# Optimization experiments

Measured on AMD Instinct MI355X. Metric: run time of the kernel, lower is better.

Reference implementation:

```python
import jax, jax.numpy as jnp
import numpy as np

B = 16; SEQ_LEN = 96; PRED_LEN = 96; N_VARS = 862; D_MODEL = 512; D_FF = 1024
N_HEADS = 8; E_LAYERS = 2; D_FREQ = 512; KF_LEN = 5000; ALPHA = 0.5; TOP_P = 0.5
FREQ_DIM = SEQ_LEN // 2 + 1            # rfft bins = 49
KEY_LEN = int(np.ceil(FREQ_DIM * ALPHA))  # 25 -> y_freq in_features = 50
KERNEL = 25; NOISE_EPS = 0.01; LN_EPS = 1e-5; REVIN_EPS = 1e-5


def setup_inputs() -> dict:
    ks = iter(jax.random.split(jax.random.key(0), 64))
    def g(*shape):
        return jax.random.normal(next(ks), shape, jnp.float32) * 0.02
    z = lambda *s: jnp.zeros(s, jnp.float32)
    o = lambda *s: jnp.ones(s, jnp.float32)
    inp = {}
    inp['x_enc'] = jax.random.normal(next(ks), (B, SEQ_LEN, N_VARS), jnp.float32)
    inp['gate_noise'] = jax.random.normal(next(ks), (N_VARS,), jnp.float32)
    inp['revin_w'] = o(N_VARS); inp['revin_b'] = z(N_VARS)
    inp['fc2_w'] = g(SEQ_LEN, D_MODEL); inp['fc2_b'] = z(D_MODEL)
    inp['fc3_w'] = g(D_MODEL, PRED_LEN); inp['fc3_b'] = z(PRED_LEN)
    inp['fc4_w'] = g(SEQ_LEN, D_MODEL); inp['fc4_b'] = z(D_MODEL)
    inp['fc5_w'] = g(D_MODEL, PRED_LEN); inp['fc5_b'] = z(PRED_LEN)
    inp['tc_w1'] = g(D_MODEL, D_MODEL // 2); inp['tc_w2'] = g(D_MODEL // 2, N_VARS)
    inp['tn_w1'] = g(D_MODEL, D_MODEL // 2); inp['tn_w2'] = g(D_MODEL // 2, N_VARS)
    inp['lt_w1'] = g(SEQ_LEN, D_MODEL); inp['lt_b1'] = z(D_MODEL)
    inp['lt_w2'] = g(D_MODEL, D_MODEL); inp['lt_b2'] = z(D_MODEL)
    inp['yf_w'] = g(2 * KEY_LEN, D_FREQ); inp['yf_b'] = z(D_FREQ)
    inp['ls_w1'] = g(D_FREQ, D_FREQ); inp['ls_b1'] = z(D_FREQ)
    inp['ls_w2'] = g(D_FREQ, D_FREQ); inp['ls_b2'] = z(D_FREQ)
    inp['fco_w'] = g(2 * D_MODEL, PRED_LEN); inp['fco_b'] = z(PRED_LEN)
    inp['freq_table'] = jax.random.normal(next(ks), (KF_LEN, N_VARS), jnp.float32)
    inp['enc_wq'] = g(E_LAYERS, D_MODEL, D_MODEL); inp['enc_bq'] = z(E_LAYERS, D_MODEL)
    inp['enc_wk'] = g(E_LAYERS, D_MODEL, D_MODEL); inp['enc_bk'] = z(E_LAYERS, D_MODEL)
    inp['enc_wv'] = g(E_LAYERS, D_MODEL, D_MODEL); inp['enc_bv'] = z(E_LAYERS, D_MODEL)
    inp['enc_wo'] = g(E_LAYERS, D_MODEL, D_MODEL); inp['enc_bo'] = z(E_LAYERS, D_MODEL)
    inp['enc_c1w'] = g(E_LAYERS, D_MODEL, D_FF); inp['enc_c1b'] = z(E_LAYERS, D_FF)
    inp['enc_c2w'] = g(E_LAYERS, D_FF, D_MODEL); inp['enc_c2b'] = z(E_LAYERS, D_MODEL)
    inp['enc_g1'] = o(E_LAYERS, D_MODEL); inp['enc_be1'] = z(E_LAYERS, D_MODEL)
    inp['enc_g2'] = o(E_LAYERS, D_MODEL); inp['enc_be2'] = z(E_LAYERS, D_MODEL)
    inp['norm_g'] = o(D_MODEL); inp['norm_b'] = z(D_MODEL)
    inp['batch_key_frequency'] = jax.random.randint(next(ks), (B,), 0, KF_LEN)
    return inp


def _lrelu(t):
    return jnp.where(t >= 0, t, 0.01 * t)


def _layernorm(x, g, b):
    m = jnp.mean(x, -1, keepdims=True)
    v = jnp.mean((x - m) ** 2, -1, keepdims=True)
    return (x - m) * jax.lax.rsqrt(v + LN_EPS) * g + b


def _decomp(x):
    # moving_avg(kernel=25, stride=1) with edge replication padding, via cumsum
    pad = (KERNEL - 1) // 2
    xp = jnp.concatenate([jnp.repeat(x[:, :1], pad, axis=1), x,
                          jnp.repeat(x[:, -1:], pad, axis=1)], axis=1)
    c = jnp.cumsum(xp, axis=1)
    c = jnp.concatenate([jnp.zeros_like(c[:, :1]), c], axis=1)
    mean = (c[:, KERNEL:] - c[:, :-KERNEL]) / KERNEL  # [B, L, N]
    return x - mean, mean


def _kf_gather(table, index, length):
    # data[(index[:,None] + arange(length)) % KF_LEN] -> [B, length, N]
    gi = (index[:, None] + jnp.arange(length)[None, :]) % KF_LEN
    return table[gi]


def _forward(x_enc, gate_noise, revin_w, revin_b, fc2_w, fc2_b, fc3_w, fc3_b,
             fc4_w, fc4_b, fc5_w, fc5_b, tc_w1, tc_w2, tn_w1, tn_w2,
             lt_w1, lt_b1, lt_w2, lt_b2, yf_w, yf_b, ls_w1, ls_b1, ls_w2, ls_b2,
             fco_w, fco_b, freq_table, enc_wq, enc_bq, enc_wk, enc_bk, enc_wv, enc_bv,
             enc_wo, enc_bo, enc_c1w, enc_c1b, enc_c2w, enc_c2b,
             enc_g1, enc_be1, enc_g2, enc_be2, norm_g, norm_b, batch_key_frequency):
    # RevIN norm (stats detached, as in RevIN)
    mean = jax.lax.stop_gradient(jnp.mean(x_enc, axis=1, keepdims=True))
    std = jax.lax.stop_gradient(jnp.sqrt(jnp.var(x_enc, axis=1, keepdims=True) + REVIN_EPS))
    x = (x_enc - mean) / std * revin_w + revin_b  # [B, L, N]

    # ---- Frequency encoder ----
    _, trend = _decomp(x)
    t = _lrelu(trend.transpose(0, 2, 1) @ lt_w1 + lt_b1) @ lt_w2 + lt_b2  # [B,N,D]
    xf = jnp.fft.rfft(x.transpose(0, 2, 1), axis=-1, norm='ortho')  # [B,N,FREQ_DIM]
    y_key = jnp.concatenate([xf.real[..., :KEY_LEN], xf.imag[..., :KEY_LEN]], axis=-1)
    y_key = y_key @ yf_w + yf_b  # [B,N,D_FREQ]
    y_key = y_key.transpose(0, 2, 1) - _kf_gather(freq_table, batch_key_frequency, D_FREQ)
    y = _lrelu(y_key.transpose(0, 2, 1) @ ls_w1 + ls_b1) @ ls_w2 + ls_b2  # [B,N,D_FREQ]
    y = y.transpose(0, 2, 1) + _kf_gather(freq_table, (batch_key_frequency + D_FREQ) % KF_LEN, D_FREQ)
    y = y.transpose(0, 2, 1)  # [B,N,D_FREQ], real part of frequency coeffs
    x_fre = jnp.fft.irfft(y.astype(jnp.complex64), n=SEQ_LEN, axis=-1, norm='ortho')  # [B,N,L]
    x_fre = x_fre @ fc4_w + fc4_b + t  # [B,N,D]
    x_fre_loss = x_fre @ fc5_w + fc5_b  # [B,N,pred]

    # ---- Time encoder ----
    xb = x.transpose(0, 2, 1) @ fc2_w + fc2_b  # [B,N,D]
    # noisy top-p gating mask
    xc = jax.nn.relu(xb @ tc_w1) @ tc_w2
    xn = jax.nn.relu(xb @ tn_w1) @ tn_w2
    # nn.Softplus(beta=-1): -log(1+exp(-x)) = -softplus(-x)
    xe = xc + gate_noise * (-jax.nn.softplus(-(xn + NOISE_EPS)))
    xmin = jnp.min(xe, axis=-1, keepdims=True)
    xmax = jnp.max(xe, axis=-1, keepdims=True)
    logits = (xe - xmin) / (xmax - xmin + 1e-6) + jnp.eye(N_VARS, dtype=xe.dtype)
    mask = (logits < TOP_P)[:, None]  # [B,1,N,N], True = masked out

    scale = 1.0 / np.sqrt(D_MODEL // N_HEADS)
    for l in range(E_LAYERS):
        q = (xb @ enc_wq[l] + enc_bq[l]).reshape(B, N_VARS, N_HEADS, -1)
        k = (xb @ enc_wk[l] + enc_bk[l]).reshape(B, N_VARS, N_HEADS, -1)
        v = (xb @ enc_wv[l] + enc_bv[l]).reshape(B, N_VARS, N_HEADS, -1)
        s = jnp.einsum('blhe,bshe->bhls', q, k)
        s = jnp.where(mask, -jnp.inf, s)
        a = jax.nn.softmax(scale * s, axis=-1)
        o = jnp.einsum('bhls,bshd->blhd', a, v).reshape(B, N_VARS, D_MODEL)
        xb = xb + (o @ enc_wo[l] + enc_bo[l])
        xb = _layernorm(xb, enc_g1[l], enc_be1[l])
        yff = jax.nn.gelu(xb @ enc_c1w[l] + enc_c1b[l], approximate=False) @ enc_c2w[l] + enc_c2b[l]
        xb = _layernorm(xb + yff, enc_g2[l], enc_be2[l])
    xb = _layernorm(xb, norm_g, norm_b)
    x_time_loss = xb @ fc3_w + fc3_b  # [B,N,pred]

    dec = (jnp.concatenate([xb, x_fre], axis=-1) @ fco_w + fco_b).transpose(0, 2, 1)  # [B,pred,N]

    def _denorm(z):
        return ((z - revin_b) / (revin_w + REVIN_EPS * REVIN_EPS)) * std + mean

    dec = _denorm(dec)
    x_time_loss = _denorm(x_time_loss.transpose(0, 2, 1))
    x_fre_loss = _denorm(x_fre_loss.transpose(0, 2, 1))
    return dec[:, -PRED_LEN:, :], x_time_loss, x_fre_loss


def reference(x_enc, gate_noise, revin_w, revin_b, fc2_w, fc2_b, fc3_w, fc3_b,
              fc4_w, fc4_b, fc5_w, fc5_b, tc_w1, tc_w2, tn_w1, tn_w2,
              lt_w1, lt_b1, lt_w2, lt_b2, yf_w, yf_b, ls_w1, ls_b1, ls_w2, ls_b2,
              fco_w, fco_b, freq_table, enc_wq, enc_bq, enc_wk, enc_bk, enc_wv, enc_bv,
              enc_wo, enc_bo, enc_c1w, enc_c1b, enc_c2w, enc_c2b,
              enc_g1, enc_be1, enc_g2, enc_be2, norm_g, norm_b, batch_key_frequency):
    return _forward(x_enc, gate_noise, revin_w, revin_b, fc2_w, fc2_b, fc3_w, fc3_b,
                    fc4_w, fc4_b, fc5_w, fc5_b, tc_w1, tc_w2, tn_w1, tn_w2,
                    lt_w1, lt_b1, lt_w2, lt_b2, yf_w, yf_b, ls_w1, ls_b1, ls_w2, ls_b2,
                    fco_w, fco_b, freq_table, enc_wq, enc_bq, enc_wk, enc_bk, enc_wv, enc_bv,
                    enc_wo, enc_bo, enc_c1w, enc_c1b, enc_c2w, enc_c2b,
                    enc_g1, enc_be1, enc_g2, enc_be2, norm_g, norm_b, batch_key_frequency)
```

## Files before the change

kernel.cpp:

```cpp
#include <hip/hip_runtime.h>
#include <hip/hip_bf16.h>
#include <math.h>

typedef __hip_bfloat16 bf16;
typedef unsigned long long u64;
using s8v = __attribute__((ext_vector_type(8))) short;
using f4v = __attribute__((ext_vector_type(4))) float;

#define B_   16
#define L_   96
#define NV   862
#define DM   512
#define NH   8
#define DH   64
#define KFL  5000
#define NBN  (B_*NV)
#define NVP  896
#define QKVW 1536
#define L2P  128

#define BAR()  __builtin_amdgcn_s_barrier()
#define SCB()  __builtin_amdgcn_sched_barrier(0)
#define VMW0() asm volatile("s_waitcnt vmcnt(0)" ::: "memory")
#define VMW4() asm volatile("s_waitcnt vmcnt(4)" ::: "memory")
#define VMW6() asm volatile("s_waitcnt vmcnt(6)" ::: "memory")
#define VMW8() asm volatile("s_waitcnt vmcnt(8)" ::: "memory")

__device__ __forceinline__ float tof(bf16 x)  { return __bfloat162float(x); }

__device__ __forceinline__ int sxl(int r, int c) {
    return (r << 6) + ((c ^ (r & 7)) << 3);
}
__device__ __forceinline__ int px(int r, int k) {
    return (r << 6) + (((((k >> 3) ^ (r & 7)) + ((r & 8) >> 2)) & 7) << 3) + (k & 7);
}
__device__ __forceinline__ int pxc(int r, int c) {
    return (r << 6) + ((((c ^ (r & 7)) + ((r & 8) >> 2)) & 7) << 3);
}

__device__ __forceinline__ void gl16(const bf16* g, bf16* l)
{
    __builtin_amdgcn_global_load_lds(
        (const __attribute__((address_space(1))) void*)g,
        (__attribute__((address_space(3))) void*)l, 16, 0, 0);
}

__device__ __forceinline__ void stage64(const bf16* __restrict__ src, int ld,
                                        int r0, int rmax, int k0, bf16* buf, int tid)
{
    #pragma unroll
    for (int i = 0; i < 2; i++) {
        int e = tid + i * 256;
        int r = e >> 3, c = e & 7;
        int gr = r0 + r; gr = gr > rmax ? rmax : gr;
        int gk = k0 + ((c ^ (r & 7)) << 3);
        gl16(src + (size_t)gr * ld + gk, buf + ((size_t)(e >> 6) << 9));
    }
}
__device__ __forceinline__ void stage128(const bf16* __restrict__ src, int ld,
                                         int r0, int rmax, int k0, bf16* buf, int tid)
{
    #pragma unroll
    for (int i = 0; i < 4; i++) {
        int e = tid + i * 256;
        int r = e >> 3, c = e & 7;
        int gr = r0 + r; gr = gr > rmax ? rmax : gr;
        int gk = k0 + ((c ^ (r & 7)) << 3);
        gl16(src + (size_t)gr * ld + gk, buf + ((size_t)(e >> 6) << 9));
    }
}

__device__ __forceinline__ int xcd_swz(int orig, int nwg)
{
    int q = nwg >> 3, r = nwg & 7;
    int xc = orig & 7, loc = orig >> 3;
    return (xc < r ? xc * (q + 1) : r * (q + 1) + (xc - r) * q) + loc;
}

__global__ void detect_k(const unsigned short* __restrict__ rw, int* __restrict__ flag)
{
    if (threadIdx.x == 0 && blockIdx.x == 0)
        *flag = (rw[0] == 0 && rw[2] == 0 && rw[4] == 0) ? 1 : 0;
}

struct CB { const void* src[30]; bf16* dst[30]; int n[30]; int so[30]; };
__global__ __launch_bounds__(256)
void cvtb_k(CB cb, const int* __restrict__ flag)
{
    int t = blockIdx.y;
    int i = blockIdx.x * 256 + threadIdx.x;
    if (i >= cb.n[t]) return;
    int s = cb.so[t] + i;
    if (*flag) cb.dst[t][i] = __float2bfloat16(((const float*)cb.src[t])[s]);
    else       cb.dst[t][i] = ((const bf16*)cb.src[t])[s];
}

#define NWT 24
struct WD { const void* src; bf16* dst; int K, Kp, N; long srcOff; };
struct WTB { WD d[NWT]; };
__global__ __launch_bounds__(256)
void wtcb_k(WTB wb, const int* __restrict__ flag)
{
    __shared__ bf16 tile[32][33];
    WD dd = wb.d[blockIdx.z];
    int n0 = blockIdx.x * 32, k0 = blockIdx.y * 32;
    if (n0 >= dd.N || k0 >= dd.Kp) return;
    int tx = threadIdx.x & 31, ty = threadIdx.x >> 5;
    int f32 = *flag;
    #pragma unroll
    for (int r = 0; r < 4; r++) {
        int k = k0 + ty + r * 8, n = n0 + tx;
        bf16 v = __float2bfloat16(0.f);
        if (k < dd.K && n < dd.N)
            v = f32 ? __float2bfloat16(((const float*)dd.src)[dd.srcOff + (size_t)k * dd.N + n])
                    : ((const bf16*)dd.src)[dd.srcOff + (size_t)k * dd.N + n];
        tile[ty + r * 8][tx] = v;
    }
    __syncthreads();
    #pragma unroll
    for (int r = 0; r < 4; r++) {
        int n = n0 + ty + r * 8, k = k0 + tx;
        if (n < dd.N && k < dd.Kp) dd.dst[(size_t)n * dd.Kp + k] = tile[tx][ty + r * 8];
    }
}

__global__ __launch_bounds__(256)
void vt_k(const bf16* __restrict__ qkv, bf16* __restrict__ Vt)
{
    __shared__ bf16 t[32][33];
    int bh = blockIdx.z;
    int n0 = blockIdx.x * 32, d0 = blockIdx.y * 32;
    int b = bh >> 3, h = bh & 7;
    int tx = threadIdx.x & 31, ty = threadIdx.x >> 5;
    #pragma unroll
    for (int r = 0; r < 4; r++) {
        int n = n0 + ty + r * 8, d = d0 + tx;
        bf16 v = __float2bfloat16(0.f);
        if (n < NV) v = qkv[(size_t)(b * NV + n) * QKVW + 1024 + h * DH + d];
        t[ty + r * 8][tx] = v;
    }
    __syncthreads();
    #pragma unroll
    for (int r = 0; r < 4; r++) {
        int d = d0 + ty + r * 8, n = n0 + tx;
        Vt[((size_t)bh * DH + d) * NVP + n] = t[tx][ty + r * 8];
    }
}

__global__ __launch_bounds__(128)
void revin_k(const void* __restrict__ x_enc, const bf16* __restrict__ rw,
             const bf16* __restrict__ rb, bf16* __restrict__ xT,
             bf16* __restrict__ trend, float* __restrict__ meanA,
             float* __restrict__ stdA, const int* __restrict__ flag)
{
    int row = blockIdx.x;
    int b = row / NV, n = row - b * NV;
    int tid = threadIdx.x;
    int f32 = *flag;
    __shared__ float xr[96];
    __shared__ float part[2][2];
    __shared__ float mv[2];
    float v = 0.f;
    if (tid < 96) {
        size_t idx = ((size_t)b * L_ + tid) * NV + n;
        v = f32 ? ((const float*)x_enc)[idx] : tof(((const bf16*)x_enc)[idx]);
    }
    float s = v, sq = v * v;
    #pragma unroll
    for (int off = 32; off; off >>= 1) {
        s  += __shfl_xor(s,  off, 64);
        sq += __shfl_xor(sq, off, 64);
    }
    int wid = tid >> 6;
    if ((tid & 63) == 0) { part[wid][0] = s; part[wid][1] = sq; }
    __syncthreads();
    if (tid == 0) {
        float S = part[0][0] + part[1][0], Q = part[0][1] + part[1][1];
        float m = S / 96.f;
        float var = fmaxf(Q / 96.f - m * m, 0.f);
        float st = sqrtf(var + 1e-5f);
        mv[0] = m; mv[1] = st;
        meanA[row] = m; stdA[row] = st;
    }
    __syncthreads();
    float m = mv[0], st = mv[1];
    const bf16 z16 = __float2bfloat16(0.f);
    if (tid < 96) {
        float xv = (v - m) / st * tof(rw[n]) + tof(rb[n]);
        xr[tid] = xv;
        xT[(size_t)row * L2P + tid] = __float2bfloat16(xv);
    } else {
        xT[(size_t)row * L2P + tid] = z16;
    }
    __syncthreads();
    if (tid < 96) {
        float acc = 0.f;
        #pragma unroll
        for (int d = -12; d <= 12; d++) {
            int k = tid + d;
            k = k < 0 ? 0 : (k > 95 ? 95 : k);
            acc += xr[k];
        }
        trend[(size_t)row * L2P + tid] = __float2bfloat16(acc * (1.f / 25.f));
    } else {
        trend[(size_t)row * L2P + tid] = z16;
    }
}

__global__ void myf_k(const bf16* __restrict__ yf_w, bf16* __restrict__ MyfT)
{
    int idx = blockIdx.x * 256 + threadIdx.x;
    if (idx >= 512 * L2P) return;
    int d = idx >> 7, l = idx & 127;
    const float invs = 0.10206207261596575f;
    float acc = 0.f;
    if (l < 96) {
        for (int f = 0; f < 25; f++) {
            float ang = (float)(f * l) / 48.0f;
            acc += cospif(ang) * tof(yf_w[f * 512 + d]);
            acc -= sinpif(ang) * tof(yf_w[(25 + f) * 512 + d]);
        }
        acc *= invs;
    }
    MyfT[(size_t)d * L2P + l] = __float2bfloat16(acc);
}

__global__ void ceff_k(const bf16* __restrict__ fc4_w, bf16* __restrict__ CeffT)
{
    int idx = blockIdx.x * 256 + threadIdx.x;
    if (idx >= 512 * 64) return;
    int d = idx >> 6, f = idx & 63;
    const float invs = 0.10206207261596575f;
    float acc = 0.f;
    if (f < 49) {
        for (int l = 0; l < 96; l++) {
            float coef;
            if (f == 0)       coef = 1.f;
            else if (f == 48) coef = (l & 1) ? -1.f : 1.f;
            else              coef = 2.f * cospif((float)(f * l) / 48.f);
            acc += coef * tof(fc4_w[l * 512 + d]);
        }
        acc *= invs;
    }
    CeffT[(size_t)d * 64 + f] = __float2bfloat16(acc);
}

__device__ __forceinline__ float epi(float v, int n, int m, int N, int act,
                                     const bf16* bias, const float* Res,
                                     const void* ft, const int* kf,
                                     const int* dflag)
{
    if (act >= 5) {
        v += tof(bias[n]);
        int b = m / NV, nv = m - b * NV;
        int gi = (act == 5) ? (kf[b] + n) % KFL : (kf[b] + 512 + n) % KFL;
        size_t gidx = (size_t)gi * NV + nv;
        float fv = (*dflag) ? ((const float*)ft)[gidx] : tof(((const bf16*)ft)[gidx]);
        return (act == 5) ? v - fv : v + fv;
    }
    if (act == 4) {
        float z = -(v + 0.01f);
        float sp = fmaxf(z, 0.f) + log1pf(expf(-fabsf(z)));
        return Res[(size_t)m * N + n] + tof(bias[n]) * (-sp);
    }
    if (bias) v += tof(bias[n]);
    if (Res)  v += Res[(size_t)m * N + n];
    if (act == 1)      v = fmaxf(v, 0.f);
    else if (act == 2) v = (v >= 0.f) ? v : 0.01f * v;
    else if (act == 3) v = 0.5f * v * (1.f + erff(v * 0.70710678118654752f));
    return v;
}

__global__ __launch_bounds__(256)
void gemm128c(const bf16* __restrict__ A, int lda,
              const bf16* __restrict__ Wt, int ldb,
              const bf16* __restrict__ bias, const float* Res,
              float* C32, bf16* C16, int M, int N, int K, int act,
              int gx, int ntile)
{
    __shared__ __align__(16) bf16 As[2][128 * 64];
    __shared__ __align__(16) bf16 Bs[2][128 * 64];
    int tid = threadIdx.x;
    int w = tid >> 6, lane = tid & 63;
    int lr = lane >> 4, lc = lane & 15;
    int nblk = gridDim.x;
    int sb = xcd_swz(blockIdx.x, nblk);
    int mq = (w >> 1) * 64, nq = (w & 1) * 64;
    int ntk = K >> 6;
    int nmine = (ntile - 1 - sb) / nblk + 1;
    int S = nmine * ntk;
    f4v acc[4][4] = {};
    const f4v z4 = {0.f, 0.f, 0.f, 0.f};

    auto SSTEP = [&](int s, int buf) {
        int tt = (s / ntk) * nblk + sb;
        int bx = tt % gx, by = tt / gx;
        int k0 = (s % ntk) << 6;
        stage128(A, lda, by * 128, M - 1, k0, As[buf], tid);
        stage128(Wt, ldb, bx * 128, N - 1, k0, Bs[buf], tid);
    };

    SSTEP(0, 0);
    if (S > 1) { SSTEP(1, 1); VMW8(); } else { VMW0(); }
    BAR(); SCB();

    for (int s = 0; s < S; s++) {
        int cur = s & 1;
        #pragma unroll
        for (int sub = 0; sub < 2; sub++) {
            int ck = sub * 4 + lr;
            s8v a[4], b[4];
            #pragma unroll
            for (int mt = 0; mt < 4; mt++) a[mt] = *(const s8v*)&As[cur][sxl(mq + mt * 16 + lc, ck)];
            #pragma unroll
            for (int j = 0; j < 4; j++) b[j] = *(const s8v*)&Bs[cur][sxl(nq + j * 16 + lc, ck)];
            #pragma unroll
            for (int mt = 0; mt < 4; mt++)
                #pragma unroll
                for (int j = 0; j < 4; j++)
                    acc[mt][j] = __builtin_amdgcn_mfma_f32_16x16x32_bf16(a[mt], b[j], acc[mt][j], 0, 0, 0);
        }
        if (s + 1 < S) {
            SCB(); BAR(); SCB();
            if (s + 2 < S) {
                SSTEP(s + 2, cur);
                VMW8();
            } else {
                VMW0();
            }
            BAR(); SCB();
        }
        if ((s % ntk) == ntk - 1) {
            int tt = (s / ntk) * nblk + sb;
            int bx = tt % gx, by = tt / gx;
            int row0 = by * 128, col0 = bx * 128;
            #pragma unroll
            for (int mt = 0; mt < 4; mt++)
            #pragma unroll
            for (int j = 0; j < 4; j++) {
                #pragma unroll
                for (int r = 0; r < 4; r++) {
                    int m = row0 + mq + mt * 16 + lr * 4 + r;
                    int n = col0 + nq + j * 16 + lc;
                    if (m >= M || n >= N) continue;
                    float v = epi(acc[mt][j][r], n, m, N, act, bias, Res, nullptr, nullptr, nullptr);
                    if (C32) C32[(size_t)m * N + n] = v;
                    if (C16) C16[(size_t)m * N + n] = __float2bfloat16(v);
                }
            }
            #pragma unroll
            for (int mt = 0; mt < 4; mt++)
                #pragma unroll
                for (int j = 0; j < 4; j++) acc[mt][j] = z4;
        }
    }
}

__global__ __launch_bounds__(256)
void gemm64c(const bf16* __restrict__ A, int lda,
             const bf16* __restrict__ Wt, int ldb,
             const bf16* __restrict__ bias, const float* Res,
             float* C32, bf16* C16, int M, int N, int K, int act,
             const void* ft, const int* kf, const int* dflag,
             int gx, int ntile)
{
    __shared__ __align__(16) bf16 As[2][64 * 64];
    __shared__ __align__(16) bf16 Bs[2][128 * 64];
    int tid = threadIdx.x;
    int w = tid >> 6, lane = tid & 63;
    int lr = lane >> 4, lc = lane & 15;
    int nblk = gridDim.x;
    int sb = xcd_swz(blockIdx.x, nblk);
    int mq = (w >> 1) * 32, nq = (w & 1) * 64;
    int ntk = K >> 6;
    int nmine = (ntile - 1 - sb) / nblk + 1;
    int S = nmine * ntk;
    f4v acc[2][4] = {};
    const f4v z4 = {0.f, 0.f, 0.f, 0.f};

    auto SSTEP = [&](int s, int buf) {
        int tt = (s / ntk) * nblk + sb;
        int bx = tt % gx, by = tt / gx;
        int k0 = (s % ntk) << 6;
        stage64(A, lda, by * 64, M - 1, k0, As[buf], tid);
        stage128(Wt, ldb, bx * 128, N - 1, k0, Bs[buf], tid);
    };

    SSTEP(0, 0);
    if (S > 1) { SSTEP(1, 1); VMW6(); } else { VMW0(); }
    BAR(); SCB();

    for (int s = 0; s < S; s++) {
        int cur = s & 1;
        #pragma unroll
        for (int sub = 0; sub < 2; sub++) {
            int ck = sub * 4 + lr;
            s8v a[2], b[4];
            #pragma unroll
            for (int mt = 0; mt < 2; mt++) a[mt] = *(const s8v*)&As[cur][sxl(mq + mt * 16 + lc, ck)];
            #pragma unroll
            for (int j = 0; j < 4; j++) b[j] = *(const s8v*)&Bs[cur][sxl(nq + j * 16 + lc, ck)];
            #pragma unroll
            for (int mt = 0; mt < 2; mt++)
                #pragma unroll
                for (int j = 0; j < 4; j++)
                    acc[mt][j] = __builtin_amdgcn_mfma_f32_16x16x32_bf16(a[mt], b[j], acc[mt][j], 0, 0, 0);
        }
        if (s + 1 < S) {
            SCB(); BAR(); SCB();
            if (s + 2 < S) {
                SSTEP(s + 2, cur);
                VMW6();
            } else {
                VMW0();
            }
            BAR(); SCB();
        }
        if ((s % ntk) == ntk - 1) {
            int tt = (s / ntk) * nblk + sb;
            int bx = tt % gx, by = tt / gx;
            int row0 = by * 64, col0 = bx * 128;
            #pragma unroll
            for (int mt = 0; mt < 2; mt++)
            #pragma unroll
            for (int j = 0; j < 4; j++) {
                #pragma unroll
                for (int r = 0; r < 4; r++) {
                    int m = row0 + mq + mt * 16 + lr * 4 + r;
                    int n = col0 + nq + j * 16 + lc;
                    if (m >= M || n >= N) continue;
                    float v = epi(acc[mt][j][r], n, m, N, act, bias, Res, ft, kf, dflag);
                    if (C32) C32[(size_t)m * N + n] = v;
                    if (C16) C16[(size_t)m * N + n] = __float2bfloat16(v);
                }
            }
            #pragma unroll
            for (int mt = 0; mt < 2; mt++)
                #pragma unroll
                for (int j = 0; j < 4; j++) acc[mt][j] = z4;
        }
    }
}

__global__ __launch_bounds__(256)
void outg_mfma(const bf16* __restrict__ xb16, const bf16* __restrict__ xfre16,
               const bf16* __restrict__ fcoT, const bf16* __restrict__ fc3T,
               const bf16* __restrict__ fc5T, const bf16* __restrict__ fcob,
               const bf16* __restrict__ fc3b, const bf16* __restrict__ fc5b,
               const bf16* __restrict__ rw, const bf16* __restrict__ rb,
               const float* __restrict__ meanA, const float* __restrict__ stdA,
               void* __restrict__ outv, const int* __restrict__ flag)
{
    __shared__ __align__(16) bf16 As[2][64 * 64];
    __shared__ __align__(16) bf16 Bs[2][64 * 64];
    const int M = NBN, N = 96;
    const size_t OSZ = (size_t)B_ * L_ * NV;
    int z = blockIdx.z;
    const bf16 *A1, *W1, *A2 = nullptr, *W2 = nullptr, *bias;
    int ldb; size_t obase;
    if (z == 0) { A1 = xb16; W1 = fcoT; A2 = xfre16; W2 = fcoT + 512; ldb = 1024; bias = fcob; obase = 0; }
    else if (z == 1) { A1 = xb16; W1 = fc3T; ldb = 512; bias = fc3b; obase = OSZ; }
    else { A1 = xfre16; W1 = fc5T; ldb = 512; bias = fc5b; obase = 2 * OSZ; }
    int tid = threadIdx.x;
    int w = tid >> 6, lane = tid & 63;
    int lr = lane >> 4, lc = lane & 15;
    int row0 = blockIdx.y * 64, col0 = blockIdx.x * 64;
    int mq = (w >> 1) * 32, nq = (w & 1) * 32;
    int f32o = *flag;
    f4v acc[2][2] = {};
    int nt = (z == 0) ? 16 : 8;
    stage64(A1, 512, row0, M - 1, 0, As[0], tid);
    stage64(W1, ldb, col0, N - 1, 0, Bs[0], tid);
    stage64(A1, 512, row0, M - 1, 64, As[1], tid);
    stage64(W1, ldb, col0, N - 1, 64, Bs[1], tid);
    VMW4();
    BAR(); SCB();
    for (int t = 0; t < nt; t++) {
        int cur = t & 1;
        #pragma unroll
        for (int sub = 0; sub < 2; sub++) {
            int ck = sub * 4 + lr;
            s8v a0 = *(const s8v*)&As[cur][sxl(mq + lc, ck)];
            s8v a1 = *(const s8v*)&As[cur][sxl(mq + 16 + lc, ck)];
            s8v b0 = *(const s8v*)&Bs[cur][sxl(nq + lc, ck)];
            s8v b1 = *(const s8v*)&Bs[cur][sxl(nq + 16 + lc, ck)];
            acc[0][0] = __builtin_amdgcn_mfma_f32_16x16x32_bf16(a0, b0, acc[0][0], 0, 0, 0);
            acc[0][1] = __builtin_amdgcn_mfma_f32_16x16x32_bf16(a0, b1, acc[0][1], 0, 0, 0);
            acc[1][0] = __builtin_amdgcn_mfma_f32_16x16x32_bf16(a1, b0, acc[1][0], 0, 0, 0);
            acc[1][1] = __builtin_amdgcn_mfma_f32_16x16x32_bf16(a1, b1, acc[1][1], 0, 0, 0);
        }
        if (t + 1 < nt) {
            SCB(); BAR(); SCB();
            if (t + 2 < nt) {
                int tn = t + 2;
                const bf16* Ax = (z == 0 && tn >= 8) ? A2 : A1;
                const bf16* Wx = (z == 0 && tn >= 8) ? W2 : W1;
                stage64(Ax, 512, row0, M - 1, (tn & 7) << 6, As[cur], tid);
                stage64(Wx, ldb, col0, N - 1, (tn & 7) << 6, Bs[cur], tid);
                VMW4();
            } else {
                VMW0();
            }
            BAR(); SCB();
        }
    }
    #pragma unroll
    for (int mt = 0; mt < 2; mt++)
    #pragma unroll
    for (int j = 0; j < 2; j++) {
        #pragma unroll
        for (int r = 0; r < 4; r++) {
            int m = row0 + mq + mt * 16 + lr * 4 + r;
            int c = col0 + nq + j * 16 + lc;
            if (m >= M || c >= N) continue;
            int b = m / NV, n = m - b * NV;
            float v = acc[mt][j][r] + tof(bias[c]);
            v = (v - tof(rb[n])) / (tof(rw[n]) + 1e-10f) * stdA[m] + meanA[m];
            size_t oidx = obase + ((size_t)b * L_ + c) * NV + n;
            if (f32o) ((float*)outv)[oidx] = v;
            else      ((bf16*)outv)[oidx] = __float2bfloat16(v);
        }
    }
}

__global__ __launch_bounds__(256)
void gating_k(const float* __restrict__ xe, u64* __restrict__ mask64)
{
    int row = blockIdx.x;
    int i = row % NV;
    int tid = threadIdx.x;
    size_t base = (size_t)row * NV;
    float vals[4];
    int cnt = 0;
    float mn = INFINITY, mx = -INFINITY;
    for (int j = tid; j < NV; j += 256) {
        float e = xe[base + j];
        vals[cnt++] = e;
        mn = fminf(mn, e);
        mx = fmaxf(mx, e);
    }
    #pragma unroll
    for (int off = 32; off; off >>= 1) {
        mn = fminf(mn, __shfl_xor(mn, off, 64));
        mx = fmaxf(mx, __shfl_xor(mx, off, 64));
    }
    __shared__ float smn[4], smx[4], fin[2];
    int w = tid >> 6, lane = tid & 63;
    if (lane == 0) { smn[w] = mn; smx[w] = mx; }
    __syncthreads();
    if (tid == 0) {
        float a = fminf(fminf(smn[0], smn[1]), fminf(smn[2], smn[3]));
        float c = fmaxf(fmaxf(smx[0], smx[1]), fmaxf(smx[2], smx[3]));
        fin[0] = a;
        fin[1] = 1.f / (c - a + 1e-6f);
    }
    __syncthreads();
    float a = fin[0], inv = fin[1];
    cnt = 0;
    for (int t = w; t < 14; t += 4) {
        int j = t * 64 + lane;
        bool masked = true;
        if (j < NV) {
            float lg = (vals[cnt++] - a) * inv + ((j == i) ? 1.f : 0.f);
            masked = (lg < 0.5f);
        }
        u64 word = __ballot(masked);
        if (lane == 0) mask64[(size_t)row * 16 + t] = word;
    }
}

__global__ __launch_bounds__(256)
void ln_k(const float* __restrict__ X, const bf16* __restrict__ g,
          const bf16* __restrict__ bta, float* __restrict__ Y32,
          bf16* __restrict__ Y16)
{
    int row = blockIdx.x;
    int tid = threadIdx.x;
    size_t base = (size_t)row * DM;
    float v0 = X[base + tid], v1 = X[base + tid + 256];
    float s = v0 + v1, sq = v0 * v0 + v1 * v1;
    #pragma unroll
    for (int off = 32; off; off >>= 1) {
        s  += __shfl_xor(s,  off, 64);
        sq += __shfl_xor(sq, off, 64);
    }
    __shared__ float ps[4], pq[4], mv[2];
    int wid = tid >> 6;
    if ((tid & 63) == 0) { ps[wid] = s; pq[wid] = sq; }
    __syncthreads();
    if (tid == 0) {
        float S = ps[0] + ps[1] + ps[2] + ps[3];
        float Q = pq[0] + pq[1] + pq[2] + pq[3];
// ... 26 lines not shown
        float s = v0 + v1, sq = v0 * v0 + v1 * v1;
        #pragma unroll
        for (int off = 32; off; off >>= 1) {
            s  += __shfl_xor(s,  off, 64);
            sq += __shfl_xor(sq, off, 64);
        }
        if ((tid & 63) == 0) { ps[wid] = s; pq[wid] = sq; }
        __syncthreads();
        if (tid == 0) {
            float S = ps[0] + ps[1] + ps[2] + ps[3];
            float Q = pq[0] + pq[1] + pq[2] + pq[3];
            float m = S / 512.f;
            float var = fmaxf(Q / 512.f - m * m, 0.f);
            mv[0] = m; mv[1] = rsqrtf(var + 1e-5f);
        }
        __syncthreads();
    }
    float m1 = mv[0], r1 = mv[1];
    float y0 = (v0 - m1) * r1 * tof(g1[tid])       + tof(b1[tid]);
    float y1 = (v1 - m1) * r1 * tof(g1[tid + 256]) + tof(b1[tid + 256]);
    __syncthreads();
    {
        float s = y0 + y1, sq = y0 * y0 + y1 * y1;
        #pragma unroll
        for (int off = 32; off; off >>= 1) {
            s  += __shfl_xor(s,  off, 64);
            sq += __shfl_xor(sq, off, 64);
        }
        if ((tid & 63) == 0) { ps[wid] = s; pq[wid] = sq; }
        __syncthreads();
        if (tid == 0) {
            float S = ps[0] + ps[1] + ps[2] + ps[3];
            float Q = pq[0] + pq[1] + pq[2] + pq[3];
            float m = S / 512.f;
            float var = fmaxf(Q / 512.f - m * m, 0.f);
            mv[0] = m; mv[1] = rsqrtf(var + 1e-5f);
        }
        __syncthreads();
    }
    float m2 = mv[0], r2 = mv[1];
    Y16[base + tid]       = __float2bfloat16((y0 - m2) * r2 * tof(g2[tid])       + tof(b2[tid]));
    Y16[base + tid + 256] = __float2bfloat16((y1 - m2) * r2 * tof(g2[tid + 256]) + tof(b2[tid + 256]));
}

__global__ __launch_bounds__(256)
void attn_k(const bf16* __restrict__ qkv, const bf16* __restrict__ Vt,
            const u64* __restrict__ mask64, bf16* __restrict__ O)
{
    __shared__ __align__(16) bf16 Ks[2][64 * 64];
    __shared__ __align__(16) bf16 Vs[2][64 * 64];
    __shared__ bf16 Pt[4][16 * 64];
    int bid = blockIdx.x;
    int bh = bid & 127;
    int q0 = (bid >> 7) * 64;
    int b = bh >> 3, h = bh & 7;
    int tid = threadIdx.x;
    int w = tid >> 6, lane = tid & 63;
    int lr = lane >> 4, lc = lane & 15;
    size_t hb = (size_t)h * DH;
    int qw = q0 + w * 16;
    const float C = 0.18033688011112042f;

    s8v qf[2];
    #pragma unroll
    for (int sub = 0; sub < 2; sub++) {
        int gq = qw + lc;
        uint4 v = make_uint4(0, 0, 0, 0);
        if (gq < NV)
            v = *(const uint4*)(qkv + ((size_t)(b * NV + gq)) * QKVW + hb + sub * 32 + lr * 8);
        qf[sub] = *(s8v*)&v;
    }

    const bf16* kbase = qkv + (size_t)b * NV * QKVW + 512 + hb;
    const bf16* vbase = Vt + (size_t)bh * DH * NVP;

    float lsum[4] = {0.f, 0.f, 0.f, 0.f};
    f4v oacc[4] = {};
    const int NT = 14;

    stage64(kbase, QKVW, 0, NV - 1, 0, Ks[0], tid);
    stage64(vbase, NVP, 0, DH - 1, 0, Vs[0], tid);
    stage64(kbase, QKVW, 64, NV - 1, 0, Ks[1], tid);
    stage64(vbase, NVP, 0, DH - 1, 64, Vs[1], tid);
    VMW4();
    BAR(); SCB();

    for (int t = 0; t < NT; t++) {
        int cur = t & 1;
        f4v s[4];
        __builtin_amdgcn_s_setprio(1);
        #pragma unroll
        for (int nt = 0; nt < 4; nt++) {
            f4v sacc = {0.f, 0.f, 0.f, 0.f};
            #pragma unroll
            for (int sub = 0; sub < 2; sub++) {
                s8v bb = *(const s8v*)&Ks[cur][sxl(nt * 16 + lc, sub * 4 + lr)];
                sacc = __builtin_amdgcn_mfma_f32_16x16x32_bf16(qf[sub], bb, sacc, 0, 0, 0);
            }
            s[nt] = sacc;
        }
        __builtin_amdgcn_s_setprio(0);
        #pragma unroll
        for (int r = 0; r < 4; r++) {
            int gq = qw + lr * 4 + r;
            u64 wd = (gq < NV) ? mask64[(size_t)(b * NV + gq) * 16 + t] : ~0ull;
            #pragma unroll
            for (int nt = 0; nt < 4; nt++) {
                float p = ((wd >> (nt * 16 + lc)) & 1) ? 0.f : exp2f(s[nt][r] * C);
                Pt[w][px(lr * 4 + r, nt * 16 + lc)] = __float2bfloat16(p);
                lsum[r] += p;
            }
        }
        #pragma unroll
        for (int sub = 0; sub < 2; sub++) {
            s8v pa = *(const s8v*)&Pt[w][pxc(lc, sub * 4 + lr)];
            __builtin_amdgcn_s_setprio(1);
            #pragma unroll
            for (int dt = 0; dt < 4; dt++) {
                s8v vv = *(const s8v*)&Vs[cur][sxl(dt * 16 + lc, sub * 4 + lr)];
                oacc[dt] = __builtin_amdgcn_mfma_f32_16x16x32_bf16(pa, vv, oacc[dt], 0, 0, 0);
            }
            __builtin_amdgcn_s_setprio(0);
        }
        if (t + 1 < NT) {
            SCB(); BAR(); SCB();
            if (t + 2 < NT) {
                int j2 = (t + 2) * 64;
                stage64(kbase, QKVW, j2, NV - 1, 0, Ks[cur], tid);
                stage64(vbase, NVP, 0, DH - 1, j2, Vs[cur], tid);
                VMW4();
            } else {
                VMW0();
            }
            BAR(); SCB();
        }
    }
    #pragma unroll
    for (int r = 0; r < 4; r++) {
        #pragma unroll
        for (int o2 = 1; o2 < 16; o2 <<= 1) lsum[r] += __shfl_xor(lsum[r], o2, 64);
    }
    #pragma unroll
    for (int r = 0; r < 4; r++) {
        int gq = qw + lr * 4 + r;
        if (gq >= NV) continue;
        float linv = 1.f / fmaxf(lsum[r], 1e-30f);
        #pragma unroll
        for (int dt = 0; dt < 4; dt++)
            O[((size_t)(b * NV + gq)) * DM + hb + dt * 16 + lc] =
                __float2bfloat16(oacc[dt][r] * linv);
    }
}

static void G1(hipStream_t s, const bf16* A, int lda, const bf16* Wt, int ldb,
               const bf16* bias, const float* Res, float* C32, bf16* C16,
               int M, int N, int K, int act)
{
    int gx = (N + 127) / 128, gy = (M + 127) / 128;
    int ntile = gx * gy;
    int nblk = ntile < 512 ? ntile : 512;
    gemm128c<<<dim3(nblk), 256, 0, s>>>(A, lda, Wt, ldb, bias, Res, C32, C16,
                                        M, N, K, act, gx, ntile);
}
static void G64(hipStream_t s, const bf16* A, int lda, const bf16* Wt, int ldb,
                const bf16* bias, const float* Res, float* C32, bf16* C16,
                int M, int N, int K, int act,
                const void* ft = nullptr, const int* kf = nullptr, const int* df = nullptr)
{
    int gx = (N + 127) / 128, gy = (M + 63) / 64;
    int ntile = gx * gy;
    int nblk = ntile < 768 ? ntile : 768;
    gemm64c<<<dim3(nblk), 256, 0, s>>>(A, lda, Wt, ldb, bias, Res, C32, C16,
                                       M, N, K, act, ft, kf, df, gx, ntile);
}

enum { I_XENC = 0, I_GNOISE, I_RW, I_RB, I_FC2W, I_FC2B, I_FC3W, I_FC3B,
       I_FC4W, I_FC4B, I_FC5W, I_FC5B, I_TCW1, I_TCW2, I_TNW1, I_TNW2,
       I_LTW1, I_LTB1, I_LTW2, I_LTB2, I_YFW, I_YFB, I_LSW1, I_LSB1,
       I_LSW2, I_LSB2, I_FCOW, I_FCOB, I_FT, I_EWQ, I_EBQ, I_EWK, I_EBK,
       I_EWV, I_EBV, I_EWO, I_EBO, I_C1W, I_C1B, I_C2W, I_C2B,
       I_G1, I_BE1, I_G2, I_BE2, I_NG, I_NB };

extern "C" void kernel_launch(void* const* d_in, const int* in_sizes, int n_in,
                              void* d_out, int out_size, void* d_ws, size_t ws_size,
                              hipStream_t stream)
{
    const int* bkey = (const int*)d_in[47];
    (void)ws_size; (void)in_sizes; (void)n_in; (void)out_size;

    float* ws = (float*)d_ws;
    size_t off = 0;
    auto alloc = [&](size_t nf) { nf = (nf + 3) & ~(size_t)3; float* p = ws + off; off += nf; return p; };
    auto balloc = [&](size_t nb) { return (bf16*)alloc((nb + 1) / 2); };
    int*  flag  = (int*)alloc(16);
    bf16* gnoise = balloc(862); bf16* rw = balloc(862); bf16* rb = balloc(862);
    bf16* fc2b = balloc(512);  bf16* fc3b = balloc(96);
    bf16* fc4w_c = balloc(49152); bf16* fc4b = balloc(512); bf16* fc5b = balloc(96);
    bf16* ltb1 = balloc(512);  bf16* ltb2 = balloc(512);
    bf16* yfw_c = balloc(25600); bf16* yfb = balloc(512);
    bf16* lsb1 = balloc(512);  bf16* lsb2 = balloc(512);
    bf16* fcob = balloc(96);
    bf16* qkvb = balloc(2 * QKVW);
    bf16* ebo = balloc(1024);  bf16* c1b = balloc(2048); bf16* c2b = balloc(1024);
    bf16* g1v = balloc(1024);  bf16* be1v = balloc(1024);
    bf16* g2v = balloc(1024);  bf16* be2v = balloc(1024);
    bf16* ngv = balloc(512);   bf16* nbv = balloc(512);
    bf16* fc2wT = balloc(512 * L2P);  bf16* fc3wT = balloc(49152); bf16* fc5wT = balloc(49152);
    bf16* lt1T = balloc(512 * L2P);   bf16* lt2T = balloc(262144);
    bf16* ls1T = balloc(262144);  bf16* ls2T = balloc(262144);
    bf16* fcoT = balloc(98304);
    bf16* tc2T = balloc(220672);  bf16* tn2T = balloc(220672);
    bf16* gate1w = balloc(262144);
    bf16* qkvw = balloc(2 * QKVW * 512);
    bf16* woT = balloc(524288);
    bf16* c1T = balloc(1048576);  bf16* c2T = balloc(1048576);
    bf16* xT    = balloc((size_t)NBN * L2P);
    bf16* trend = balloc((size_t)NBN * L2P);
    float* meanA = alloc(13824);
    float* stdA  = alloc(13824);
    bf16* MyfT  = balloc(512 * L2P);
    bf16* CeffT = balloc(512 * 64);
    bf16* y49   = balloc((size_t)NBN * 64);
    float* xb32 = alloc((size_t)NBN * 512);
    bf16* xb16  = balloc((size_t)NBN * 512);
    bf16* xfre16 = balloc((size_t)NBN * 512);
    bf16* tmp16 = balloc((size_t)NBN * 1024);
    float* fbuf = alloc((size_t)NBN * 512);
    float* gbuf = alloc((size_t)NBN * 1024);
    u64* mask64 = (u64*)alloc((size_t)NBN * 32);

    float* xe = gbuf;
    bf16* yA  = (bf16*)gbuf;
    bf16* qkv16 = (bf16*)gbuf;
    bf16* O16 = qkv16 + (size_t)NBN * QKVW;
    bf16* Vt  = tmp16;

    detect_k<<<1, 64, 0, stream>>>((const unsigned short*)d_in[I_RW], flag);

    {
        CB cb;
        int k = 0;
        auto add = [&](int idx, bf16* dst, int n, int so) {
            cb.src[k] = d_in[idx]; cb.dst[k] = dst; cb.n[k] = n; cb.so[k] = so; k++;
        };
        add(I_GNOISE, gnoise, 862, 0); add(I_RW, rw, 862, 0); add(I_RB, rb, 862, 0);
        add(I_FC2B, fc2b, 512, 0); add(I_FC3B, fc3b, 96, 0);
        add(I_FC4W, fc4w_c, 49152, 0); add(I_FC4B, fc4b, 512, 0); add(I_FC5B, fc5b, 96, 0);
        add(I_LTB1, ltb1, 512, 0); add(I_LTB2, ltb2, 512, 0);
        add(I_YFW, yfw_c, 25600, 0); add(I_YFB, yfb, 512, 0);
        add(I_LSB1, lsb1, 512, 0); add(I_LSB2, lsb2, 512, 0);
        add(I_FCOB, fcob, 96, 0);
        add(I_EBQ, qkvb + 0, 512, 0);          add(I_EBQ, qkvb + QKVW, 512, 512);
        add(I_EBK, qkvb + 512, 512, 0);        add(I_EBK, qkvb + QKVW + 512, 512, 512);
        add(I_EBV, qkvb + 1024, 512, 0);       add(I_EBV, qkvb + QKVW + 1024, 512, 512);
        add(I_EBO, ebo, 1024, 0); add(I_C1B, c1b, 2048, 0); add(I_C2B, c2b, 1024, 0);
        add(I_G1, g1v, 1024, 0); add(I_BE1, be1v, 1024, 0);
        add(I_G2, g2v, 1024, 0); add(I_BE2, be2v, 1024, 0);
        add(I_NG, ngv, 512, 0); add(I_NB, nbv, 512, 0);
        cvtb_k<<<dim3(192, 30), 256, 0, stream>>>(cb, flag);
    }

    {
        WTB wb;
        int k = 0;
        auto add = [&](int idx, bf16* dst, int K, int Kp, int N, long soff) {
            wb.d[k].src = d_in[idx]; wb.d[k].dst = dst;
            wb.d[k].K = K; wb.d[k].Kp = Kp; wb.d[k].N = N; wb.d[k].srcOff = soff; k++;
        };
        add(I_FC2W, fc2wT, 96, L2P, 512, 0);
        add(I_FC3W, fc3wT, 512, 512, 96, 0);
        add(I_FC5W, fc5wT, 512, 512, 96, 0);
        add(I_LTW1, lt1T, 96, L2P, 512, 0);
        add(I_LTW2, lt2T, 512, 512, 512, 0);
        add(I_LSW1, ls1T, 512, 512, 512, 0);
        add(I_LSW2, ls2T, 512, 512, 512, 0);
        add(I_FCOW, fcoT, 1024, 1024, 96, 0);
        add(I_TCW2, tc2T, 256, 256, 862, 0);
        add(I_TNW2, tn2T, 256, 256, 862, 0);
        add(I_TCW1, gate1w, 512, 512, 256, 0);
        add(I_TNW1, gate1w + 256 * 512, 512, 512, 256, 0);
        for (int l = 0; l < 2; l++) {
            add(I_EWO, woT + (size_t)l * 262144, 512, 512, 512, (long)l * 262144);
            add(I_C1W, c1T + (size_t)l * 524288, 512, 512, 1024, (long)l * 524288);
            add(I_C2W, c2T + (size_t)l * 524288, 1024, 1024, 512, (long)l * 524288);
            add(I_EWQ, qkvw + (size_t)l * 786432 + 0,      512, 512, 512, (long)l * 262144);
            add(I_EWK, qkvw + (size_t)l * 786432 + 262144, 512, 512, 512, (long)l * 262144);
            add(I_EWV, qkvw + (size_t)l * 786432 + 524288, 512, 512, 512, (long)l * 262144);
        }
        wtcb_k<<<dim3(32, 32, NWT), 256, 0, stream>>>(wb, flag);
    }

    revin_k<<<NBN, 128, 0, stream>>>(d_in[I_XENC], rw, rb, xT, trend, meanA, stdA, flag);
    myf_k<<<(512 * L2P + 255) / 256, 256, 0, stream>>>(yfw_c, MyfT);
    ceff_k<<<(512 * 64 + 255) / 256, 256, 0, stream>>>(fc4w_c, CeffT);

    G64(stream, trend, L2P, lt1T, L2P, ltb1, nullptr, nullptr, tmp16, NBN, 512, L2P, 2);
    G64(stream, tmp16, 512, lt2T, 512, ltb2, nullptr, fbuf, nullptr, NBN, 512, 512, 0);
    G64(stream, xT, L2P, MyfT, L2P, yfb, nullptr, nullptr, yA, NBN, 512, L2P, 5,
        d_in[I_FT], bkey, flag);
    G64(stream, yA, 512, ls1T, 512, lsb1, nullptr, nullptr, tmp16, NBN, 512, 512, 2);
    G64(stream, tmp16, 512, ls2T, 512, lsb2, nullptr, nullptr, y49, NBN, 64, 512, 6,
        d_in[I_FT], bkey, flag);
    G64(stream, y49, 64, CeffT, 64, fc4b, fbuf, nullptr, xfre16, NBN, 512, 64, 0);

    G64(stream, xT, L2P, fc2wT, L2P, fc2b, nullptr, xb32, xb16, NBN, 512, L2P, 0);

    G64(stream, xb16, 512, gate1w, 512, nullptr, nullptr, nullptr, tmp16, NBN, 512, 512, 1);
    G64(stream, tmp16, 512, tc2T, 256, nullptr, nullptr, xe, nullptr, NBN, 862, 256, 0);
    G64(stream, tmp16 + 256, 512, tn2T, 256, gnoise, xe, xe, nullptr, NBN, 862, 256, 4);
    gating_k<<<NBN, 256, 0, stream>>>(xe, mask64);

    for (int l = 0; l < 2; l++) {
        G1(stream, xb16, 512, qkvw + (size_t)l * QKVW * 512, 512,
           qkvb + l * QKVW, nullptr, nullptr, qkv16, NBN, QKVW, 512, 0);
        vt_k<<<dim3(NVP / 32, DH / 32, B_ * NH), 256, 0, stream>>>(qkv16, Vt);
        attn_k<<<dim3(14 * 128), 256, 0, stream>>>(qkv16, Vt, mask64, O16);
        G64(stream, O16, 512, woT + (size_t)l * 262144, 512, ebo + l * 512,
            xb32, fbuf, nullptr, NBN, 512, 512, 0);
        ln_k<<<NBN, 256, 0, stream>>>(fbuf, g1v + l * 512, be1v + l * 512, xb32, xb16);
        G1(stream, xb16, 512, c1T + (size_t)l * 524288, 512, c1b + l * 1024,
           nullptr, nullptr, tmp16, NBN, 1024, 512, 3);
        G64(stream, tmp16, 1024, c2T + (size_t)l * 524288, 1024, c2b + l * 512,
            xb32, fbuf, nullptr, NBN, 512, 1024, 0);
        if (l == 0)
            ln_k<<<NBN, 256, 0, stream>>>(fbuf, g2v, be2v, xb32, xb16);
        else
            ln2x_k<<<NBN, 256, 0, stream>>>(fbuf, g2v + 512, be2v + 512, ngv, nbv, xb16);
    }

    outg_mfma<<<dim3(2, (NBN + 63) / 64, 3), 256, 0, stream>>>(
        xb16, xfre16, fcoT, fc3wT, fc5wT, fcob, fc3b, fc5b,
        rw, rb, meanA, stdA, d_out, flag);
}
```

Baseline: 1.612 ms.

## Replace both GEMM kernels with a single 256x256-tile 512-thread MFMA kernel

Merges the 128x128 and 64x128 persistent GEMM kernels into one kernel. It uses 256x256 output tiles, 8 waves of 512 threads, 128 KB of double-buffered LDS and 4x8 MFMA accumulators per wave. The goal is more operand reuse per LDS load and fewer global loads per output element. The risk is the tile count: with M≈13.8k and N=512 only about 108 tiles exist, fewer than the number of CUs. The N=64 and N=862 GEMMs also waste padded work, and register pressure goes up.

```diff
diff --git a/kernel.cpp b/kernel.cpp
--- a/kernel.cpp
+++ b/kernel.cpp
@@ -23,7 +23,6 @@
 #define SCB()  __builtin_amdgcn_sched_barrier(0)
 #define VMW0() asm volatile("s_waitcnt vmcnt(0)" ::: "memory")
 #define VMW4() asm volatile("s_waitcnt vmcnt(4)" ::: "memory")
-#define VMW6() asm volatile("s_waitcnt vmcnt(6)" ::: "memory")
 #define VMW8() asm volatile("s_waitcnt vmcnt(8)" ::: "memory")
 
 __device__ __forceinline__ float tof(bf16 x)  { return __bfloat162float(x); }
@@ -57,12 +56,12 @@
         gl16(src + (size_t)gr * ld + gk, buf + ((size_t)(e >> 6) << 9));
     }
 }
-__device__ __forceinline__ void stage128(const bf16* __restrict__ src, int ld,
-                                         int r0, int rmax, int k0, bf16* buf, int tid)
+__device__ __forceinline__ void stage256w(const bf16* __restrict__ src, int ld,
+                                          int r0, int rmax, int k0, bf16* buf, int tid)
 {
     #pragma unroll
     for (int i = 0; i < 4; i++) {
-        int e = tid + i * 256;
+        int e = tid + i * 512;
         int r = e >> 3, c = e & 7;
         int gr = r0 + r; gr = gr > rmax ? rmax : gr;
         int gk = k0 + ((c ^ (r & 7)) << 3);
@@ -271,33 +270,35 @@
     return v;
 }
 
-__global__ __launch_bounds__(256)
-void gemm128c(const bf16* __restrict__ A, int lda,
-              const bf16* __restrict__ Wt, int ldb,
-              const bf16* __restrict__ bias, const float* Res,
-              float* C32, bf16* C16, int M, int N, int K, int act,
-              int gx, int ntile)
-{
-    __shared__ __align__(16) bf16 As[2][128 * 64];
-    __shared__ __align__(16) bf16 Bs[2][128 * 64];
+__global__ __launch_bounds__(512, 2)
+void gemmP(const bf16* __restrict__ A, int lda,
+           const bf16* __restrict__ Wt, int ldb,
+           const bf16* __restrict__ bias, const float* Res,
+           float* C32, bf16* C16, int M, int N, int K, int act,
+           const void* ft, const int* kf, const int* dflag,
+           int gx, int ntile)
+{
+    __shared__ __align__(16) bf16 As[2][256 * 64];
+    __shared__ __align__(16) bf16 Bs[2][256 * 64];
     int tid = threadIdx.x;
     int w = tid >> 6, lane = tid & 63;
     int lr = lane >> 4, lc = lane & 15;
     int nblk = gridDim.x;
     int sb = xcd_swz(blockIdx.x, nblk);
-    int mq = (w >> 1) * 64, nq = (w & 1) * 64;
+    int mq = (w >> 1) * 64;
+    int nq = (w & 1) * 128;
     int ntk = K >> 6;
     int nmine = (ntile - 1 - sb) / nblk + 1;
     int S = nmine * ntk;
-    f4v acc[4][4] = {};
+    f4v acc[4][8] = {};
     const f4v z4 = {0.f, 0.f, 0.f, 0.f};
 
     auto SSTEP = [&](int s, int buf) {
         int tt = (s / ntk) * nblk + sb;
         int bx = tt % gx, by = tt / gx;
         int k0 = (s % ntk) << 6;
-        stage128(A, lda, by * 128, M - 1, k0, As[buf], tid);
-        stage128(Wt, ldb, bx * 128, N - 1, k0, Bs[buf], tid);
+        stage256w(A, lda, by * 256, M - 1, k0, As[buf], tid);
+        stage256w(Wt, ldb, bx * 256, N - 1, k0, Bs[buf], tid);
     };
 
     SSTEP(0, 0);
@@ -309,15 +310,15 @@
         #pragma unroll
         for (int sub = 0; sub < 2; sub++) {
             int ck = sub * 4 + lr;
-            s8v a[4], b[4];
+            s8v a[4], b[8];
             #pragma unroll
             for (int mt = 0; mt < 4; mt++) a[mt] = *(const s8v*)&As[cur][sxl(mq + mt * 16 + lc, ck)];
             #pragma unroll
-            for (int j = 0; j < 4; j++) b[j] = *(const s8v*)&Bs[cur][sxl(nq + j * 16 + lc, ck)];
+            for (int j = 0; j < 8; j++) b[j] = *(const s8v*)&Bs[cur][sxl(nq + j * 16 + lc, ck)];
             #pragma unroll
             for (int mt = 0; mt < 4; mt++)
                 #pragma unroll
-                for (int j = 0; j < 4; j++)
+                for (int j = 0; j < 8; j++)
                     acc[mt][j] = __builtin_amdgcn_mfma_f32_16x16x32_bf16(a[mt], b[j], acc[mt][j], 0, 0, 0);
         }
         if (s + 1 < S) {
@@ -333,97 +334,11 @@
         if ((s % ntk) == ntk - 1) {
             int tt = (s / ntk) * nblk + sb;
             int bx = tt % gx, by = tt / gx;
-            int row0 = by * 128, col0 = bx * 128;
+            int row0 = by * 256, col0 = bx * 256;
             #pragma unroll
             for (int mt = 0; mt < 4; mt++)
             #pragma unroll
-            for (int j = 0; j < 4; j++) {
-                #pragma unroll
-                for (int r = 0; r < 4; r++) {
-                    int m = row0 + mq + mt * 16 + lr * 4 + r;
-                    int n = col0 + nq + j * 16 + lc;
-                    if (m >= M || n >= N) continue;
-                    float v = epi(acc[mt][j][r], n, m, N, act, bias, Res, nullptr, nullptr, nullptr);
-                    if (C32) C32[(size_t)m * N + n] = v;
-                    if (C16) C16[(size_t)m * N + n] = __float2bfloat16(v);
-                }
-            }
-            #pragma unroll
-            for (int mt = 0; mt < 4; mt++)
-                #pragma unroll
-                for (int j = 0; j < 4; j++) acc[mt][j] = z4;
-        }
-    }
-}
-
-__global__ __launch_bounds__(256)
-void gemm64c(const bf16* __restrict__ A, int lda,
-             const bf16* __restrict__ Wt, int ldb,
-             const bf16* __restrict__ bias, const float* Res,
-             float* C32, bf16* C16, int M, int N, int K, int act,
-             const void* ft, const int* kf, const int* dflag,
-             int gx, int ntile)
-{
-    __shared__ __align__(16) bf16 As[2][64 * 64];
-    __shared__ __align__(16) bf16 Bs[2][128 * 64];
-    int tid = threadIdx.x;
-    int w = tid >> 6, lane = tid & 63;
-    int lr = lane >> 4, lc = lane & 15;
-    int nblk = gridDim.x;
-    int sb = xcd_swz(blockIdx.x, nblk);
-    int mq = (w >> 1) * 32, nq = (w & 1) * 64;
-    int ntk = K >> 6;
-    int nmine = (ntile - 1 - sb) / nblk + 1;
-    int S = nmine * ntk;
-    f4v acc[2][4] = {};
-    const f4v z4 = {0.f, 0.f, 0.f, 0.f};
-
-    auto SSTEP = [&](int s, int buf) {
-        int tt = (s / ntk) * nblk + sb;
-        int bx = tt % gx, by = tt / gx;
-        int k0 = (s % ntk) << 6;
-        stage64(A, lda, by * 64, M - 1, k0, As[buf], tid);
-        stage128(Wt, ldb, bx * 128, N - 1, k0, Bs[buf], tid);
-    };
-
-    SSTEP(0, 0);
-    if (S > 1) { SSTEP(1, 1); VMW6(); } else { VMW0(); }
-    BAR(); SCB();
-
-    for (int s = 0; s < S; s++) {
-        int cur = s & 1;
-        #pragma unroll
-        for (int sub = 0; sub < 2; sub++) {
-            int ck = sub * 4 + lr;
-            s8v a[2], b[4];
-            #pragma unroll
-            for (int mt = 0; mt < 2; mt++) a[mt] = *(const s8v*)&As[cur][sxl(mq + mt * 16 + lc, ck)];
-            #pragma unroll
-            for (int j = 0; j < 4; j++) b[j] = *(const s8v*)&Bs[cur][sxl(nq + j * 16 + lc, ck)];
-            #pragma unroll
-            for (int mt = 0; mt < 2; mt++)
-                #pragma unroll
-                for (int j = 0; j < 4; j++)
-                    acc[mt][j] = __builtin_amdgcn_mfma_f32_16x16x32_bf16(a[mt], b[j], acc[mt][j], 0, 0, 0);
-        }
-        if (s + 1 < S) {
-            SCB(); BAR(); SCB();
-            if (s + 2 < S) {
-                SSTEP(s + 2, cur);
-                VMW6();
-            } else {
-                VMW0();
-            }
-            BAR(); SCB();
-        }
-        if ((s % ntk) == ntk - 1) {
-            int tt = (s / ntk) * nblk + sb;
-            int bx = tt % gx, by = tt / gx;
-            int row0 = by * 64, col0 = bx * 128;
-            #pragma unroll
-            for (int mt = 0; mt < 2; mt++)
-            #pragma unroll
-            for (int j = 0; j < 4; j++) {
+            for (int j = 0; j < 8; j++) {
                 #pragma unroll
                 for (int r = 0; r < 4; r++) {
                     int m = row0 + mq + mt * 16 + lr * 4 + r;
@@ -435,9 +350,9 @@
                 }
             }
             #pragma unroll
-            for (int mt = 0; mt < 2; mt++)
+            for (int mt = 0; mt < 4; mt++)
                 #pragma unroll
-                for (int j = 0; j < 4; j++) acc[mt][j] = z4;
+                for (int j = 0; j < 8; j++) acc[mt][j] = z4;
         }
     }
 }
@@ -770,26 +685,16 @@
     }
 }
 
-static void G1(hipStream_t s, const bf16* A, int lda, const bf16* Wt, int ldb,
+static void GP(hipStream_t s, const bf16* A, int lda, const bf16* Wt, int ldb,
                const bf16* bias, const float* Res, float* C32, bf16* C16,
-               int M, int N, int K, int act)
-{
-    int gx = (N + 127) / 128, gy = (M + 127) / 128;
+               int M, int N, int K, int act,
+               const void* ft = nullptr, const int* kf = nullptr, const int* df = nullptr)
+{
+    int gx = (N + 255) / 256, gy = (M + 255) / 256;
     int ntile = gx * gy;
-    int nblk = ntile < 512 ? ntile : 512;
-    gemm128c<<<dim3(nblk), 256, 0, s>>>(A, lda, Wt, ldb, bias, Res, C32, C16,
-                                        M, N, K, act, gx, ntile);
-}
-static void G64(hipStream_t s, const bf16* A, int lda, const bf16* Wt, int ldb,
-                const bf16* bias, const float* Res, float* C32, bf16* C16,
-                int M, int N, int K, int act,
-                const void* ft = nullptr, const int* kf = nullptr, const int* df = nullptr)
-{
-    int gx = (N + 127) / 128, gy = (M + 63) / 64;
-    int ntile = gx * gy;
-    int nblk = ntile < 768 ? ntile : 768;
-    gemm64c<<<dim3(nblk), 256, 0, s>>>(A, lda, Wt, ldb, bias, Res, C32, C16,
-                                       M, N, K, act, ft, kf, df, gx, ntile);
+    int nblk = ntile < 256 ? ntile : 256;
+    gemmP<<<dim3(nblk), 512, 0, s>>>(A, lda, Wt, ldb, bias, Res, C32, C16,
+                                     M, N, K, act, ft, kf, df, gx, ntile);
 }
 
 enum { I_XENC = 0, I_GNOISE, I_RW, I_RB, I_FC2W, I_FC2B, I_FC3W, I_FC3B,
@@ -912,34 +817,34 @@
     myf_k<<<(512 * L2P + 255) / 256, 256, 0, stream>>>(yfw_c, MyfT);
     ceff_k<<<(512 * 64 + 255) / 256, 256, 0, stream>>>(fc4w_c, CeffT);
 
-    G64(stream, trend, L2P, lt1T, L2P, ltb1, nullptr, nullptr, tmp16, NBN, 512, L2P, 2);
-    G64(stream, tmp16, 512, lt2T, 512, ltb2, nullptr, fbuf, nullptr, NBN, 512, 512, 0);
-    G64(stream, xT, L2P, MyfT, L2P, yfb, nullptr, nullptr, yA, NBN, 512, L2P, 5,
-        d_in[I_FT], bkey, flag);
-    G64(stream, yA, 512, ls1T, 512, lsb1, nullptr, nullptr, tmp16, NBN, 512, 512, 2);
-    G64(stream, tmp16, 512, ls2T, 512, lsb2, nullptr, nullptr, y49, NBN, 64, 512, 6,
-        d_in[I_FT], bkey, flag);
-    G64(stream, y49, 64, CeffT, 64, fc4b, fbuf, nullptr, xfre16, NBN, 512, 64, 0);
-
-    G64(stream, xT, L2P, fc2wT, L2P, fc2b, nullptr, xb32, xb16, NBN, 512, L2P, 0);
-
-    G64(stream, xb16, 512, gate1w, 512, nullptr, nullptr, nullptr, tmp16, NBN, 512, 512, 1);
-    G64(stream, tmp16, 512, tc2T, 256, nullptr, nullptr, xe, nullptr, NBN, 862, 256, 0);
-    G64(stream, tmp16 + 256, 512, tn2T, 256, gnoise, xe, xe, nullptr, NBN, 862, 256, 4);
+    GP(stream, trend, L2P, lt1T, L2P, ltb1, nullptr, nullptr, tmp16, NBN, 512, L2P, 2);
+    GP(stream, tmp16, 512, lt2T, 512, ltb2, nullptr, fbuf, nullptr, NBN, 512, 512, 0);
+    GP(stream, xT, L2P, MyfT, L2P, yfb, nullptr, nullptr, yA, NBN, 512, L2P, 5,
+       d_in[I_FT], bkey, flag);
+    GP(stream, yA, 512, ls1T, 512, lsb1, nullptr, nullptr, tmp16, NBN, 512, 512, 2);
+    GP(stream, tmp16, 512, ls2T, 512, lsb2, nullptr, nullptr, y49, NBN, 64, 512, 6,
+       d_in[I_FT], bkey, flag);
+    GP(stream, y49, 64, CeffT, 64, fc4b, fbuf, nullptr, xfre16, NBN, 512, 64, 0);
+
+    GP(stream, xT, L2P, fc2wT, L2P, fc2b, nullptr, xb32, xb16, NBN, 512, L2P, 0);
+
+    GP(stream, xb16, 512, gate1w, 512, nullptr, nullptr, nullptr, tmp16, NBN, 512, 512, 1);
+    GP(stream, tmp16, 512, tc2T, 256, nullptr, nullptr, xe, nullptr, NBN, 862, 256, 0);
+    GP(stream, tmp16 + 256, 512, tn2T, 256, gnoise, xe, xe, nullptr, NBN, 862, 256, 4);
     gating_k<<<NBN, 256, 0, stream>>>(xe, mask64);
 
     for (int l = 0; l < 2; l++) {
-        G1(stream, xb16, 512, qkvw + (size_t)l * QKVW * 512, 512,
+        GP(stream, xb16, 512, qkvw + (size_t)l * QKVW * 512, 512,
            qkvb + l * QKVW, nullptr, nullptr, qkv16, NBN, QKVW, 512, 0);
         vt_k<<<dim3(NVP / 32, DH / 32, B_ * NH), 256, 0, stream>>>(qkv16, Vt);
         attn_k<<<dim3(14 * 128), 256, 0, stream>>>(qkv16, Vt, mask64, O16);
-        G64(stream, O16, 512, woT + (size_t)l * 262144, 512, ebo + l * 512,
-            xb32, fbuf, nullptr, NBN, 512, 512, 0);
+        GP(stream, O16, 512, woT + (size_t)l * 262144, 512, ebo + l * 512,
+           xb32, fbuf, nullptr, NBN, 512, 512, 0);
         ln_k<<<NBN, 256, 0, stream>>>(fbuf, g1v + l * 512, be1v + l * 512, xb32, xb16);
-        G1(stream, xb16, 512, c1T + (size_t)l * 524288, 512, c1b + l * 1024,
+        GP(stream, xb16, 512, c1T + (size_t)l * 524288, 512, c1b + l * 1024,
            nullptr, nullptr, tmp16, NBN, 1024, 512, 3);
-        G64(stream, tmp16, 1024, c2T + (size_t)l * 524288, 1024, c2b + l * 512,
-            xb32, fbuf, nullptr, NBN, 512, 1024, 0);
+        GP(stream, tmp16, 1024, c2T + (size_t)l * 524288, 1024, c2b + l * 512,
+           xb32, fbuf, nullptr, NBN, 512, 1024, 0);
         if (l == 0)
             ln_k<<<NBN, 256, 0, stream>>>(fbuf, g2v, be2v, xb32, xb16);
         else
```

Measured after the change: 5.290 ms. +228.2%, slower.
